# Kernel tuning notes

Measured on AMD Instinct MI355X. Metric: run time of the kernel, lower is better.

Reference implementation:

```python
import jax, jax.numpy as jnp
import numpy as np


def setup_inputs() -> dict:
    key = jax.random.key(0)
    k1, k2 = jax.random.split(key)
    B, D, T = 8, 64, 8192
    K = 1024
    z = jax.random.normal(k1, (B, D, T), dtype=jnp.float32)
    # nn.init.uniform_(-1/K, 1/K)
    codebook = jax.random.uniform(k2, (K, D), dtype=jnp.float32,
                                  minval=-1.0 / K, maxval=1.0 / K)
    return {"z": z, "codebook": codebook}


def reference(z, codebook):
    # z: [B, D, T], codebook: [K, D]
    z_t = jnp.transpose(z, (0, 2, 1))  # [B, T, D]
    # squared L2 distances: ||z||^2 + ||e||^2 - 2 z.e  -> [B, T, K]
    d = (jnp.sum(z_t * z_t, axis=-1, keepdims=True)
         + jnp.sum(codebook * codebook, axis=-1)
         - 2.0 * jnp.einsum('btd,kd->btk', z_t, codebook))
    codes = jnp.argmin(d, axis=-1)  # [B, T] int
    quantized = jnp.transpose(codebook[codes], (0, 2, 1))  # [B, D, T]
    # straight-through estimator
    quantized_st = z + jax.lax.stop_gradient(quantized - z)
    commit_loss = jnp.mean((jax.lax.stop_gradient(quantized) - z) ** 2)
    return codes, quantized_st, commit_loss
```

## Files before the change

kernel.cpp:

```cpp
#include <hip/hip_runtime.h>
#include <hip/hip_bf16.h>

typedef __attribute__((ext_vector_type(8))) short short8;
typedef __attribute__((ext_vector_type(4))) float f32x4;

constexpr int Bb = 8;
constexpr int Dd = 64;
constexpr int Tt = 8192;
constexpr int Kk = 1024;
constexpr int BT = Bb * Tt;
constexpr int NTOT = Bb * Dd * Tt;

constexpr int OUT_Q_OFF = BT;
constexpr int OUT_LOSS_OFF = BT + NTOT;

constexpr size_t WS_PREC_OFF  = 0;
constexpr size_t WS_PART_OFF  = WS_PREC_OFF + 4096;
constexpr size_t WS_EI_OFF    = WS_PART_OFF + 4096;

__device__ inline ushort rne_bf16(float v) {
    unsigned u = __float_as_uint(v);
    return (ushort)((u + 0x7FFFu + ((u >> 16) & 1u)) >> 16);
}
__device__ inline float bf16f(ushort h) { return __uint_as_float(((unsigned)h) << 16); }

__global__ void __launch_bounds__(256) prep_kernel(const float* __restrict__ cb,
                                                   float* __restrict__ prec,
                                                   ushort* __restrict__ ei) {
    const int k = blockIdx.x * 256 + threadIdx.x;
    const float4* row = reinterpret_cast<const float4*>(cb + (size_t)k * Dd);
    float4 v[16];
    float s = 0.f;
#pragma unroll
    for (int i = 0; i < 16; ++i) {
        v[i] = row[i];
        s = fmaf(v[i].x, v[i].x, s); s = fmaf(v[i].y, v[i].y, s);
        s = fmaf(v[i].z, v[i].z, s); s = fmaf(v[i].w, v[i].w, s);
    }
    prec[k] = s;
#pragma unroll
    for (int g = 0; g < 8; ++g) {
        float vals[8] = {v[2*g].x, v[2*g].y, v[2*g].z, v[2*g].w,
                         v[2*g+1].x, v[2*g+1].y, v[2*g+1].z, v[2*g+1].w};
        short8 hv, mv, lv;
#pragma unroll
        for (int j = 0; j < 8; ++j) {
            float x = vals[j];
            ushort h = rne_bf16(x);  float hf = bf16f(h);
            float r1 = x - hf;       ushort m = rne_bf16(r1); float mf = bf16f(m);
            float r2 = r1 - mf;      ushort l = rne_bf16(r2);
            hv[j] = (short)h; mv[j] = (short)m; lv[j] = (short)l;
        }
        const size_t base = (size_t)k * 192 + g * 8;
        *reinterpret_cast<short8*>(ei + base + 0)   = hv;
        *reinterpret_cast<short8*>(ei + base + 64)  = mv;
        *reinterpret_cast<short8*>(ei + base + 128) = lv;
    }
}

constexpr int TM = 64;
constexpr int NKT = Kk / 64;

__global__ void __launch_bounds__(256, 2) mfma_argmin_kernel(
    const float* __restrict__ z, const float* __restrict__ cb,
    const ushort* __restrict__ ei,
    const float* __restrict__ prec, float* __restrict__ out,
    float* __restrict__ partials)
{
    __shared__ __align__(16) ushort z_lds[3 * 64 * 64];
    __shared__ float zsq_part[4][64];
    __shared__ float zsq_lds[64];
    __shared__ float red_v[4][64];
    __shared__ int   red_i[4][64];
    __shared__ int   codes_lds[64];

    const int tid = threadIdx.x;
    const int lane = tid & 63;
    const int w = tid >> 6;
    const int row0 = blockIdx.x * TM;
    const int b = row0 >> 13;
    const int t0 = row0 & (Tt - 1);

    {
        const int tt = tid & 63;
        const int dg = tid >> 6;
        const float* zp = z + (size_t)b * (Dd * Tt) + (size_t)(dg * 16) * Tt + (t0 + tt);
        float vals[16];
        float psum = 0.f;
#pragma unroll
        for (int i = 0; i < 16; ++i) {
            float v = zp[(size_t)i * Tt];
            vals[i] = v;
            psum = fmaf(v, v, psum);
        }
        zsq_part[dg][tt] = psum;
#pragma unroll
        for (int g = 0; g < 2; ++g) {
            short8 hv, mv, lv;
#pragma unroll
            for (int j = 0; j < 8; ++j) {
                float v = vals[g * 8 + j];
                ushort h = rne_bf16(v);  float hf = bf16f(h);
                float r1 = v - hf;       ushort m = rne_bf16(r1); float mf = bf16f(m);
                float r2 = r1 - mf;      ushort l = rne_bf16(r2);
                hv[j] = (short)h; mv[j] = (short)m; lv[j] = (short)l;
            }
            const int byte_in_row = dg * 32 + g * 16;
            const int sw = tt * 128 + (byte_in_row ^ ((tt & 7) << 4));
            *reinterpret_cast<short8*>((char*)z_lds + 0 * 8192 + sw) = hv;
            *reinterpret_cast<short8*>((char*)z_lds + 1 * 8192 + sw) = mv;
            *reinterpret_cast<short8*>((char*)z_lds + 2 * 8192 + sw) = lv;
        }
    }
    __syncthreads();
    if (tid < 64)
        zsq_lds[tid] = ((zsq_part[0][tid] + zsq_part[1][tid]) + zsq_part[2][tid]) + zsq_part[3][tid];
    __syncthreads();

    short8 A[3][2][4];
#pragma unroll
    for (int sA = 0; sA < 3; ++sA)
#pragma unroll
        for (int ds = 0; ds < 2; ++ds)
#pragma unroll
            for (int rf = 0; rf < 4; ++rf) {
                const int row = rf * 16 + (lane & 15);
                const int dby = ds * 64 + ((lane >> 4) * 16);
                A[sA][ds][rf] = *reinterpret_cast<const short8*>(
                    (char*)z_lds + sA * 8192 + row * 128 + (dby ^ ((row & 7) << 4)));
            }

    float zsq_r[16];
#pragma unroll
    for (int rf = 0; rf < 4; ++rf)
#pragma unroll
        for (int j = 0; j < 4; ++j)
            zsq_r[rf * 4 + j] = zsq_lds[rf * 16 + (lane >> 4) * 4 + j];

    float bestv[16];
    int   besti[16];
#pragma unroll
    for (int i = 0; i < 16; ++i) { bestv[i] = 3.4e38f; besti[i] = 0; }

    const int kl = lane & 15;
    const int d16b = (lane >> 4) * 16;

    short8 Bc[6];
    float esqc;
    {
        const size_t kg = (size_t)(w * 16 + kl);
        const char* pb = (const char*)ei + kg * 384 + d16b;
        Bc[0] = *reinterpret_cast<const short8*>(pb + 0);
        Bc[1] = *reinterpret_cast<const short8*>(pb + 64);
        Bc[2] = *reinterpret_cast<const short8*>(pb + 128);
        Bc[3] = *reinterpret_cast<const short8*>(pb + 192);
        Bc[4] = *reinterpret_cast<const short8*>(pb + 256);
        Bc[5] = *reinterpret_cast<const short8*>(pb + 320);
        esqc = prec[kg];
    }

    for (int kt = 0; kt < NKT; ++kt) {
        short8 Bn[6];
        float esqn = 0.f;
        if (kt + 1 < NKT) {
            const size_t kg = (size_t)((kt + 1) * 64 + w * 16 + kl);
            const char* pb = (const char*)ei + kg * 384 + d16b;
            Bn[0] = *reinterpret_cast<const short8*>(pb + 0);
            Bn[1] = *reinterpret_cast<const short8*>(pb + 64);
            Bn[2] = *reinterpret_cast<const short8*>(pb + 128);
            Bn[3] = *reinterpret_cast<const short8*>(pb + 192);
            Bn[4] = *reinterpret_cast<const short8*>(pb + 256);
            Bn[5] = *reinterpret_cast<const short8*>(pb + 320);
            esqn = prec[kg];
        }

        f32x4 acc[4];
#pragma unroll
        for (int rf = 0; rf < 4; ++rf) acc[rf] = (f32x4){0.f, 0.f, 0.f, 0.f};

#pragma unroll
        for (int ds = 0; ds < 2; ++ds) {
#pragma unroll
            for (int rf = 0; rf < 4; ++rf)
                acc[rf] = __builtin_amdgcn_mfma_f32_16x16x32_bf16(A[0][ds][rf], Bc[0 * 2 + ds], acc[rf], 0, 0, 0);
#pragma unroll
            for (int rf = 0; rf < 4; ++rf)
                acc[rf] = __builtin_amdgcn_mfma_f32_16x16x32_bf16(A[0][ds][rf], Bc[1 * 2 + ds], acc[rf], 0, 0, 0);
#pragma unroll
            for (int rf = 0; rf < 4; ++rf)
                acc[rf] = __builtin_amdgcn_mfma_f32_16x16x32_bf16(A[0][ds][rf], Bc[2 * 2 + ds], acc[rf], 0, 0, 0);
#pragma unroll
            for (int rf = 0; rf < 4; ++rf)
                acc[rf] = __builtin_amdgcn_mfma_f32_16x16x32_bf16(A[1][ds][rf], Bc[0 * 2 + ds], acc[rf], 0, 0, 0);
#pragma unroll
            for (int rf = 0; rf < 4; ++rf)
                acc[rf] = __builtin_amdgcn_mfma_f32_16x16x32_bf16(A[1][ds][rf], Bc[1 * 2 + ds], acc[rf], 0, 0, 0);
#pragma unroll
            for (int rf = 0; rf < 4; ++rf)
                acc[rf] = __builtin_amdgcn_mfma_f32_16x16x32_bf16(A[2][ds][rf], Bc[0 * 2 + ds], acc[rf], 0, 0, 0);
        }

        const int kglob = kt * 64 + w * 16 + kl;
#pragma unroll
        for (int rf = 0; rf < 4; ++rf)
#pragma unroll
            for (int j = 0; j < 4; ++j) {
                const float t1 = zsq_r[rf * 4 + j] + esqc;
                const float s = fmaf(-2.f, acc[rf][j], t1);
                if (s < bestv[rf * 4 + j]) { bestv[rf * 4 + j] = s; besti[rf * 4 + j] = kglob; }
            }

        if (kt + 1 < NKT) {
#pragma unroll
            for (int i = 0; i < 6; ++i) Bc[i] = Bn[i];
            esqc = esqn;
        }
    }

#pragma unroll
    for (int i = 0; i < 16; ++i) {
#pragma unroll
        for (int m = 1; m < 16; m <<= 1) {
            const float ov = __shfl_xor(bestv[i], m, 16);
            const int   oi = __shfl_xor(besti[i], m, 16);
            if (ov < bestv[i] || (ov == bestv[i] && oi < besti[i])) {
                bestv[i] = ov; besti[i] = oi;
            }
        }
    }
    if ((lane & 15) == 0) {
#pragma unroll
        for (int rf = 0; rf < 4; ++rf)
#pragma unroll
            for (int j = 0; j < 4; ++j) {
                const int row = rf * 16 + (lane >> 4) * 4 + j;
                red_v[w][row] = bestv[rf * 4 + j];
                red_i[w][row] = besti[rf * 4 + j];
            }
    }
    __syncthreads();
    if (tid < 64) {
        float bv = red_v[0][tid];
        int   bi = red_i[0][tid];
#pragma unroll
        for (int s2 = 1; s2 < 4; ++s2) {
            const float v = red_v[s2][tid];
            const int   i = red_i[s2][tid];
            if (v < bv || (v == bv && i < bi)) { bv = v; bi = i; }
        }
        codes_lds[tid] = bi;
        out[row0 + tid] = (float)bi;
    }
    __syncthreads();

    {
        const int tt = tid & 63;
        const int dg = tid >> 6;
        const int code = codes_lds[tt];
        const float4* crow = reinterpret_cast<const float4*>(cb + (size_t)code * Dd + dg * 16);
        float4 q4[4];
#pragma unroll
        for (int i = 0; i < 4; ++i) q4[i] = crow[i];
        const float qf[16] = {q4[0].x, q4[0].y, q4[0].z, q4[0].w,
                              q4[1].x, q4[1].y, q4[1].z, q4[1].w,
                              q4[2].x, q4[2].y, q4[2].z, q4[2].w,
                              q4[3].x, q4[3].y, q4[3].z, q4[3].w};
        float* obase = out + OUT_Q_OFF + (size_t)b * (Dd * Tt) + (size_t)(dg * 16) * Tt + (t0 + tt);
        float lacc = 0.f;
#pragma unroll
        for (int g = 0; g < 2; ++g) {
            const int sw = tt * 128 + ((dg * 32 + g * 16) ^ ((tt & 7) << 4));
            const short8 zh8 = *reinterpret_cast<const short8*>((char*)z_lds + 0 * 8192 + sw);
            const short8 zm8 = *reinterpret_cast<const short8*>((char*)z_lds + 1 * 8192 + sw);
            const short8 zl8 = *reinterpret_cast<const short8*>((char*)z_lds + 2 * 8192 + sw);
#pragma unroll
            for (int j = 0; j < 8; ++j) {
                const float zv = (bf16f((ushort)zh8[j]) + bf16f((ushort)zm8[j])) + bf16f((ushort)zl8[j]);
                const float qv = qf[g * 8 + j];
                const float diff = qv - zv;
                lacc = fmaf(diff, diff, lacc);
                obase[(size_t)(g * 8 + j) * Tt] = qv;
            }
        }
        float* red256 = &zsq_part[0][0];
        red256[tid] = lacc;
        __syncthreads();
#pragma unroll
        for (int s = 128; s > 0; s >>= 1) {
            if (tid < s) red256[tid] += red256[tid + s];
            __syncthreads();
        }
        if (tid == 0) partials[blockIdx.x] = red256[0];
    }
}

__global__ void __launch_bounds__(256) loss_kernel(const float* __restrict__ partials,
                                                   float* __restrict__ out) {
    __shared__ float red[256];
    const int t = threadIdx.x;
    red[t] = ((partials[t] + partials[t + 256]) + partials[t + 512]) + partials[t + 768];
    __syncthreads();
#pragma unroll
    for (int s = 128; s > 0; s >>= 1) {
        if (t < s) red[t] += red[t + s];
        __syncthreads();
    }
    if (t == 0)
        out[OUT_LOSS_OFF] = red[0] * (1.0f / (float)NTOT);
}

extern "C" void kernel_launch(void* const* d_in, const int* in_sizes, int n_in,
                              void* d_out, int out_size, void* d_ws, size_t ws_size,
                              hipStream_t stream) {
    const float* z = (const float*)d_in[0];
    const float* cb = (const float*)d_in[1];
    float* out = (float*)d_out;

    char* ws = (char*)d_ws;
    float* prec = (float*)(ws + WS_PREC_OFF);
    float* partials = (float*)(ws + WS_PART_OFF);
    ushort* ei = (ushort*)(ws + WS_EI_OFF);

    prep_kernel<<<Kk / 256, 256, 0, stream>>>(cb, prec, ei);
    mfma_argmin_kernel<<<BT / TM, 256, 0, stream>>>(z, cb, ei, prec, out, partials);
    loss_kernel<<<1, 256, 0, stream>>>(partials, out);
}
```

Measured before the change: 76.81 us.

## Switch distance GEMM to 32x32x16 MFMA with 2x2 wave tiling

Replaces the 16x16x32 bf16 MFMA tiling, where each wave covered all 64 rows and 16 codes, with 32x32x16 MFMA where waves split into a 2x2 grid of 32 rows by 32 codes. The goal is fewer MFMA issues and better operand reuse per instruction. It also halves the per-wave A fragment registers. Each wave now loads twice as many codebook fragments per iteration, the shuffle reduction widens to 32 lanes, and the cross-wave reduction drops to two partials.

```diff
diff --git a/kernel.cpp b/kernel.cpp
--- a/kernel.cpp
+++ b/kernel.cpp
@@ -2,7 +2,7 @@
 #include <hip/hip_bf16.h>
 
 typedef __attribute__((ext_vector_type(8))) short short8;
-typedef __attribute__((ext_vector_type(4))) float f32x4;
+typedef __attribute__((ext_vector_type(16))) float f32x16;
 
 constexpr int Bb = 8;
 constexpr int Dd = 64;
@@ -70,13 +70,17 @@
     __shared__ __align__(16) ushort z_lds[3 * 64 * 64];
     __shared__ float zsq_part[4][64];
     __shared__ float zsq_lds[64];
-    __shared__ float red_v[4][64];
-    __shared__ int   red_i[4][64];
+    __shared__ float red_v[2][64];
+    __shared__ int   red_i[2][64];
     __shared__ int   codes_lds[64];
 
     const int tid = threadIdx.x;
     const int lane = tid & 63;
     const int w = tid >> 6;
+    const int wr = w >> 1;
+    const int wk = w & 1;
+    const int kl32 = lane & 31;
+    const int hi = lane >> 5;
     const int row0 = blockIdx.x * TM;
     const int b = row0 >> 13;
     const int t0 = row0 & (Tt - 1);
@@ -117,102 +121,78 @@
         zsq_lds[tid] = ((zsq_part[0][tid] + zsq_part[1][tid]) + zsq_part[2][tid]) + zsq_part[3][tid];
     __syncthreads();
 
-    short8 A[3][2][4];
+    short8 A[3][4];
 #pragma unroll
     for (int sA = 0; sA < 3; ++sA)
 #pragma unroll
-        for (int ds = 0; ds < 2; ++ds)
-#pragma unroll
-            for (int rf = 0; rf < 4; ++rf) {
-                const int row = rf * 16 + (lane & 15);
-                const int dby = ds * 64 + ((lane >> 4) * 16);
-                A[sA][ds][rf] = *reinterpret_cast<const short8*>(
-                    (char*)z_lds + sA * 8192 + row * 128 + (dby ^ ((row & 7) << 4)));
-            }
+        for (int ds = 0; ds < 4; ++ds) {
+            const int row = wr * 32 + kl32;
+            const int dby = ds * 32 + hi * 16;
+            A[sA][ds] = *reinterpret_cast<const short8*>(
+                (char*)z_lds + sA * 8192 + row * 128 + (dby ^ ((row & 7) << 4)));
+        }
 
     float zsq_r[16];
 #pragma unroll
-    for (int rf = 0; rf < 4; ++rf)
-#pragma unroll
-        for (int j = 0; j < 4; ++j)
-            zsq_r[rf * 4 + j] = zsq_lds[rf * 16 + (lane >> 4) * 4 + j];
+    for (int reg = 0; reg < 16; ++reg)
+        zsq_r[reg] = zsq_lds[wr * 32 + (reg & 3) + 8 * (reg >> 2) + 4 * hi];
 
     float bestv[16];
     int   besti[16];
 #pragma unroll
     for (int i = 0; i < 16; ++i) { bestv[i] = 3.4e38f; besti[i] = 0; }
 
-    const int kl = lane & 15;
-    const int d16b = (lane >> 4) * 16;
-
-    short8 Bc[6];
+    short8 Bc[3][4];
     float esqc;
     {
-        const size_t kg = (size_t)(w * 16 + kl);
-        const char* pb = (const char*)ei + kg * 384 + d16b;
-        Bc[0] = *reinterpret_cast<const short8*>(pb + 0);
-        Bc[1] = *reinterpret_cast<const short8*>(pb + 64);
-        Bc[2] = *reinterpret_cast<const short8*>(pb + 128);
-        Bc[3] = *reinterpret_cast<const short8*>(pb + 192);
-        Bc[4] = *reinterpret_cast<const short8*>(pb + 256);
-        Bc[5] = *reinterpret_cast<const short8*>(pb + 320);
+        const size_t kg = (size_t)(wk * 32 + kl32);
+        const char* pb = (const char*)ei + kg * 384 + hi * 16;
+#pragma unroll
+        for (int p = 0; p < 3; ++p)
+#pragma unroll
+            for (int ds = 0; ds < 4; ++ds)
+                Bc[p][ds] = *reinterpret_cast<const short8*>(pb + p * 128 + ds * 32);
         esqc = prec[kg];
     }
 
     for (int kt = 0; kt < NKT; ++kt) {
-        short8 Bn[6];
+        short8 Bn[3][4];
         float esqn = 0.f;
         if (kt + 1 < NKT) {
-            const size_t kg = (size_t)((kt + 1) * 64 + w * 16 + kl);
-            const char* pb = (const char*)ei + kg * 384 + d16b;
-            Bn[0] = *reinterpret_cast<const short8*>(pb + 0);
-            Bn[1] = *reinterpret_cast<const short8*>(pb + 64);
-            Bn[2] = *reinterpret_cast<const short8*>(pb + 128);
-            Bn[3] = *reinterpret_cast<const short8*>(pb + 192);
-            Bn[4] = *reinterpret_cast<const short8*>(pb + 256);
-            Bn[5] = *reinterpret_cast<const short8*>(pb + 320);
+            const size_t kg = (size_t)((kt + 1) * 64 + wk * 32 + kl32);
+            const char* pb = (const char*)ei + kg * 384 + hi * 16;
+#pragma unroll
+            for (int p = 0; p < 3; ++p)
+#pragma unroll
+                for (int ds = 0; ds < 4; ++ds)
+                    Bn[p][ds] = *reinterpret_cast<const short8*>(pb + p * 128 + ds * 32);
             esqn = prec[kg];
         }
 
-        f32x4 acc[4];
-#pragma unroll
-        for (int rf = 0; rf < 4; ++rf) acc[rf] = (f32x4){0.f, 0.f, 0.f, 0.f};
-
-#pragma unroll
-        for (int ds = 0; ds < 2; ++ds) {
-#pragma unroll
-            for (int rf = 0; rf < 4; ++rf)
-                acc[rf] = __builtin_amdgcn_mfma_f32_16x16x32_bf16(A[0][ds][rf], Bc[0 * 2 + ds], acc[rf], 0, 0, 0);
-#pragma unroll
-            for (int rf = 0; rf < 4; ++rf)
-                acc[rf] = __builtin_amdgcn_mfma_f32_16x16x32_bf16(A[0][ds][rf], Bc[1 * 2 + ds], acc[rf], 0, 0, 0);
-#pragma unroll
-            for (int rf = 0; rf < 4; ++rf)
-                acc[rf] = __builtin_amdgcn_mfma_f32_16x16x32_bf16(A[0][ds][rf], Bc[2 * 2 + ds], acc[rf], 0, 0, 0);
-#pragma unroll
-            for (int rf = 0; rf < 4; ++rf)
-                acc[rf] = __builtin_amdgcn_mfma_f32_16x16x32_bf16(A[1][ds][rf], Bc[0 * 2 + ds], acc[rf], 0, 0, 0);
-#pragma unroll
-            for (int rf = 0; rf < 4; ++rf)
-                acc[rf] = __builtin_amdgcn_mfma_f32_16x16x32_bf16(A[1][ds][rf], Bc[1 * 2 + ds], acc[rf], 0, 0, 0);
-#pragma unroll
-            for (int rf = 0; rf < 4; ++rf)
-                acc[rf] = __builtin_amdgcn_mfma_f32_16x16x32_bf16(A[2][ds][rf], Bc[0 * 2 + ds], acc[rf], 0, 0, 0);
-        }
-
-        const int kglob = kt * 64 + w * 16 + kl;
-#pragma unroll
-        for (int rf = 0; rf < 4; ++rf)
-#pragma unroll
-            for (int j = 0; j < 4; ++j) {
-                const float t1 = zsq_r[rf * 4 + j] + esqc;
-                const float s = fmaf(-2.f, acc[rf][j], t1);
-                if (s < bestv[rf * 4 + j]) { bestv[rf * 4 + j] = s; besti[rf * 4 + j] = kglob; }
-            }
+        f32x16 acc = (f32x16)(0.f);
+
+#pragma unroll
+        for (int p = 0; p < 6; ++p) {
+            const int pa = (p < 3) ? 0 : (p < 5 ? 1 : 2);
+            const int pbs = (p < 3) ? p : (p < 5 ? p - 3 : 0);
+#pragma unroll
+            for (int ds = 0; ds < 4; ++ds)
+                acc = __builtin_amdgcn_mfma_f32_32x32x16_bf16(A[pa][ds], Bc[pbs][ds], acc, 0, 0, 0);
+        }
+
+        const int kglob = kt * 64 + wk * 32 + kl32;
+#pragma unroll
+        for (int reg = 0; reg < 16; ++reg) {
+            const float t1 = zsq_r[reg] + esqc;
+            const float s = fmaf(-2.f, acc[reg], t1);
+            if (s < bestv[reg]) { bestv[reg] = s; besti[reg] = kglob; }
+        }
 
         if (kt + 1 < NKT) {
 #pragma unroll
-            for (int i = 0; i < 6; ++i) Bc[i] = Bn[i];
+            for (int p = 0; p < 3; ++p)
+#pragma unroll
+                for (int ds = 0; ds < 4; ++ds) Bc[p][ds] = Bn[p][ds];
             esqc = esqn;
         }
     }
@@ -220,34 +200,29 @@
 #pragma unroll
     for (int i = 0; i < 16; ++i) {
 #pragma unroll
-        for (int m = 1; m < 16; m <<= 1) {
-            const float ov = __shfl_xor(bestv[i], m, 16);
-            const int   oi = __shfl_xor(besti[i], m, 16);
+        for (int m = 1; m < 32; m <<= 1) {
+            const float ov = __shfl_xor(bestv[i], m, 32);
+            const int   oi = __shfl_xor(besti[i], m, 32);
             if (ov < bestv[i] || (ov == bestv[i] && oi < besti[i])) {
                 bestv[i] = ov; besti[i] = oi;
             }
         }
     }
-    if ((lane & 15) == 0) {
-#pragma unroll
-        for (int rf = 0; rf < 4; ++rf)
-#pragma unroll
-            for (int j = 0; j < 4; ++j) {
-                const int row = rf * 16 + (lane >> 4) * 4 + j;
-                red_v[w][row] = bestv[rf * 4 + j];
-                red_i[w][row] = besti[rf * 4 + j];
-            }
+    if (kl32 == 0) {
+#pragma unroll
+        for (int reg = 0; reg < 16; ++reg) {
+            const int row_local = wr * 32 + (reg & 3) + 8 * (reg >> 2) + 4 * hi;
+            red_v[wk][row_local] = bestv[reg];
+            red_i[wk][row_local] = besti[reg];
+        }
     }
     __syncthreads();
     if (tid < 64) {
         float bv = red_v[0][tid];
         int   bi = red_i[0][tid];
-#pragma unroll
-        for (int s2 = 1; s2 < 4; ++s2) {
-            const float v = red_v[s2][tid];
-            const int   i = red_i[s2][tid];
-            if (v < bv || (v == bv && i < bi)) { bv = v; bi = i; }
-        }
+        const float v1 = red_v[1][tid];
+        const int   i1 = red_i[1][tid];
+        if (v1 < bv || (v1 == bv && i1 < bi)) { bv = v1; bi = i1; }
         codes_lds[tid] = bi;
         out[row0 + tid] = (float)bi;
     }
```

Result: slower. 115.7 us (+50.7%).
